# Kernel optimization log

Hardware: AMD Instinct MI355X
Metric: run time of the kernel (lower is better)

Reference implementation:

```python
import jax, jax.numpy as jnp
import numpy as np

ALPHA = 0.2  # LeakyReLU negative slope
NEG_INF = -9e15


def setup_inputs() -> dict:
    key = jax.random.key(0)
    k1, k2, k3, k4 = jax.random.split(key, 4)
    B, N, F_in, F_out = 8, 2048, 256, 128
    h = jax.random.normal(k1, (B, N, F_in), dtype=jnp.float32)
    adj = jax.random.randint(k2, (B, N, N), 0, 2, dtype=jnp.int32)
    # xavier_uniform with gain=1.414
    def xavier(k, shape, gain=1.414):
        fan_in, fan_out = shape[0], shape[1]
        limit = gain * np.sqrt(6.0 / (fan_in + fan_out))
        return jax.random.uniform(k, shape, jnp.float32, -limit, limit)
    W = xavier(k3, (F_in, F_out))
    a = xavier(k4, (2 * F_out, 1))
    return {"h": h, "adj": adj, "W": W, "a": a}


def reference(h, adj, W, a):
    # h: [B,N,F_in], adj: [B,N,N], W: [F_in,F_out], a: [2*F_out,1]
    Wh = jnp.einsum('bnf,fe->bne', h, W)  # [B,N,E]
    E = Wh.shape[-1]
    a_src, a_dst = a[:E, 0], a[E:, 0]
    # e[b,i,j] = leakyrelu(Wh[b,i].a_src + Wh[b,j].a_dst)  (additive decomposition
    # of a @ concat(Wh_i, Wh_j) -- same math, no [B,N,N,2E] intermediate)
    s_src = Wh @ a_src  # [B,N]
    s_dst = Wh @ a_dst  # [B,N]
    e = jax.nn.leaky_relu(s_src[:, :, None] + s_dst[:, None, :], negative_slope=ALPHA)
    e = jnp.where(adj > 0, e, NEG_INF)
    attention = jax.nn.softmax(e, axis=2)  # [B,N,N]
    # dropout p=0.0 / eval mode -> identity
    h_prime = jnp.einsum('bij,bje->bie', attention, Wh)
    return jax.nn.elu(h_prime)  # concat=True
```

## Files before the change

kernel.cpp:

```cpp
#include <hip/hip_runtime.h>
#include <hip/hip_bf16.h>

#define GAT_ALPHA 0.2f
#define LOG2E 1.4426950408889634f

typedef float f32x4 __attribute__((ext_vector_type(4)));
typedef int   i32x4 __attribute__((ext_vector_type(4)));
typedef short bf16x8 __attribute__((ext_vector_type(8)));

static constexpr int Nn  = 2048;
static constexpr int FIN = 256;
static constexpr int FO  = 128;

static __device__ __forceinline__ unsigned short f2bf(float x) {
    __hip_bfloat16 h = __float2bfloat16(x);
    return __builtin_bit_cast(unsigned short, h);
}
static __device__ __forceinline__ float bf2f(unsigned short u) {
    unsigned int v = ((unsigned int)u) << 16;
    return __builtin_bit_cast(float, v);
}

__global__ __launch_bounds__(256) void gat_prep(
        const float* __restrict__ W, const float* __restrict__ a,
        float* __restrict__ wa, unsigned int* __restrict__ md_key)
{
    __shared__ float pr[32][8];
    __shared__ float pd[32][8];
    const int t = threadIdx.x;
    const int kl = t >> 3, seg = t & 7;
    const int k = blockIdx.x * 32 + kl;
    float ps = 0.f, pv = 0.f;
    const float* wr = W + (size_t)k * FO + seg * 16;
    #pragma unroll
    for (int f = 0; f < 16; f += 4) {
        f32x4 wv = *(const f32x4*)(wr + f);
        f32x4 as = *(const f32x4*)(a + seg * 16 + f);
        f32x4 ad = *(const f32x4*)(a + FO + seg * 16 + f);
        ps += wv[0]*as[0] + wv[1]*as[1] + wv[2]*as[2] + wv[3]*as[3];
        pv += wv[0]*ad[0] + wv[1]*ad[1] + wv[2]*ad[2] + wv[3]*ad[3];
    }
    pr[kl][seg] = ps; pd[kl][seg] = pv;
    __syncthreads();
    if (t < 32) {
        float s = 0.f, d = 0.f;
        #pragma unroll
        for (int j = 0; j < 8; ++j) { s += pr[t][j]; d += pd[t][j]; }
        wa[blockIdx.x * 32 + t]       = s;
        wa[256 + blockIdx.x * 32 + t] = d;
    }
    if (blockIdx.x == 0 && t < 8) md_key[t] = 0u;
}

__global__ __launch_bounds__(256) void gat_wh(
        const float* __restrict__ h, const float* __restrict__ W,
        const float* __restrict__ wa, unsigned short* __restrict__ WhB,
        float* __restrict__ s_src, float* __restrict__ s_dst,
        unsigned int* __restrict__ md_key)
{
    __shared__ unsigned short WT[FO][264];
    __shared__ float wal[512];
    __shared__ float sred[64][4][2];
    __shared__ float red64[64];
    const int t  = threadIdx.x;
    const int b  = blockIdx.x & 7;
    const int n0 = (blockIdx.x >> 3) << 6;

    if (t < 128) *(f32x4*)&wal[t * 4] = *(const f32x4*)&wa[t * 4];
    #pragma unroll
    for (int c = 0; c < 32; ++c) {
        int flat = c * 1024 + t * 4;
        int k = flat >> 7, f = flat & 127;
        f32x4 wv = *(const f32x4*)&W[flat];
        WT[f + 0][k] = f2bf(wv[0]);
        WT[f + 1][k] = f2bf(wv[1]);
        WT[f + 2][k] = f2bf(wv[2]);
        WT[f + 3][k] = f2bf(wv[3]);
    }
    __syncthreads();

    {
        const int row = t >> 2, seg = t & 3;
        const float* hp  = h + ((size_t)(b * Nn + n0 + row)) * FIN + seg * 64;
        const float* was = &wal[seg * 64];
        const float* wad = &wal[256 + seg * 64];
        float ps = 0.f, pv = 0.f;
        #pragma unroll
        for (int j = 0; j < 64; j += 4) {
            f32x4 hv = *(const f32x4*)(hp + j);
            f32x4 sv = *(const f32x4*)(was + j);
            f32x4 dv = *(const f32x4*)(wad + j);
            ps += hv[0]*sv[0] + hv[1]*sv[1] + hv[2]*sv[2] + hv[3]*sv[3];
            pv += hv[0]*dv[0] + hv[1]*dv[1] + hv[2]*dv[2] + hv[3]*dv[3];
        }
        sred[row][seg][0] = ps;
        sred[row][seg][1] = pv;
    }
    __syncthreads();
    if (t < 64) {
        float s = sred[t][0][0] + sred[t][1][0] + sred[t][2][0] + sred[t][3][0];
        float d = sred[t][0][1] + sred[t][1][1] + sred[t][2][1] + sred[t][3][1];
        s_src[b * Nn + n0 + t] = s;
        s_dst[b * Nn + n0 + t] = d;
        red64[t] = d;
    }
    __syncthreads();
    if (t < 16) red64[t] = fmaxf(fmaxf(red64[t], red64[t + 16]),
                                 fmaxf(red64[t + 32], red64[t + 48]));
    __syncthreads();
    if (t == 0) {
        float m = red64[0];
        #pragma unroll
        for (int j = 1; j < 16; ++j) m = fmaxf(m, red64[j]);
        unsigned int bits = __builtin_bit_cast(unsigned int, m);
        unsigned int key  = (bits & 0x80000000u) ? ~bits : (bits | 0x80000000u);
        atomicMax(md_key + b, key);
    }

    const int w = t >> 6, lane = t & 63, n16 = lane & 15, quad = lane >> 4;
    const float* ha = h + ((size_t)(b * Nn + n0 + w * 16 + n16)) * FIN + quad * 8;
    f32x4 acc[8] = {};
    #pragma unroll
    for (int ks = 0; ks < 8; ++ks) {
        f32x4 h0 = *(const f32x4*)(ha + ks * 32);
        f32x4 h1 = *(const f32x4*)(ha + ks * 32 + 4);
        bf16x8 af;
        af[0] = (short)f2bf(h0[0]); af[1] = (short)f2bf(h0[1]);
        af[2] = (short)f2bf(h0[2]); af[3] = (short)f2bf(h0[3]);
        af[4] = (short)f2bf(h1[0]); af[5] = (short)f2bf(h1[1]);
        af[6] = (short)f2bf(h1[2]); af[7] = (short)f2bf(h1[3]);
        #pragma unroll
        for (int nt = 0; nt < 8; ++nt) {
            bf16x8 bfr = *(const bf16x8*)&WT[nt * 16 + n16][ks * 32 + quad * 8];
            acc[nt] = __builtin_amdgcn_mfma_f32_16x16x32_bf16(af, bfr, acc[nt], 0, 0, 0);
        }
    }
    {
        const int K   = (n0 >> 5) + (w >> 1);
        const int jl  = ((w & 1) << 4) + (quad << 2);
        const int q2  = jl >> 3;
        const int off = jl & 7;
        unsigned short* wpb = WhB + (((size_t)(b * 64 + K)) << 12)
                                  + (((q2 << 4) + n16) << 3) + off;
        #pragma unroll
        for (int nt = 0; nt < 8; ++nt) {
            ushort4 pk;
            pk.x = f2bf(acc[nt][0]); pk.y = f2bf(acc[nt][1]);
            pk.z = f2bf(acc[nt][2]); pk.w = f2bf(acc[nt][3]);
            *(ushort4*)(wpb + ((size_t)nt << 9)) = pk;
        }
    }
}

__global__ __launch_bounds__(256, 3) void gat_attn(
        const int* __restrict__ adj,
        const unsigned short* __restrict__ WhB,
        const float* __restrict__ s_src, const float* __restrict__ s_dst,
        const unsigned int* __restrict__ md_key, float* __restrict__ out)
{
    __shared__ float sdl[2048];
    __shared__ unsigned long long msk[32][34];
    __shared__ float accbuf[2][32][132];
    __shared__ float l_red[32];

    const int t = threadIdx.x, w = t >> 6, lane = t & 63;
    const int n16 = lane & 15, quad = lane >> 4;
    const int b  = blockIdx.x & 7;
    const int i0 = (blockIdx.x >> 3) << 5;

    {
        const int* ab = adj + ((size_t)(b * Nn + i0)) * Nn;
        unsigned int* mskw = (unsigned int*)&msk[0][0];
        #pragma unroll 2
        for (int s = 0; s < 8; ++s) {
            const int* p = ab + (s << 13) + (t << 5);
            unsigned int m = 0;
            #pragma unroll
            for (int c = 0; c < 8; ++c) {
                i32x4 v = *(const i32x4*)(p + (c << 2));
                m |= (v[0] > 0 ? 1u : 0u) << (c * 4 + 0);
                m |= (v[1] > 0 ? 1u : 0u) << (c * 4 + 1);
                m |= (v[2] > 0 ? 1u : 0u) << (c * 4 + 2);
                m |= (v[3] > 0 ? 1u : 0u) << (c * 4 + 3);
            }
            const int wi = (s << 8) + t;
            mskw[(wi >> 6) * 68 + (wi & 63)] = m;
        }
    }
    #pragma unroll
    for (int c = 0; c < 2; ++c) {
        int idx = (c << 10) + (t << 2);
        *(f32x4*)&sdl[idx] = *(const f32x4*)&s_dst[b * Nn + idx];
    }
    if (t < 32) l_red[t] = 0.f;
    __syncthreads();

    const unsigned int key = md_key[b];
    const unsigned int mb_ = (key & 0x80000000u) ? (key ^ 0x80000000u) : ~key;
    const float mdb = __builtin_bit_cast(float, mb_);
    float ssL[2], mi[2];
    #pragma unroll
    for (int ig = 0; ig < 2; ++ig) {
        float ss = s_src[b * Nn + i0 + (ig << 4) + n16];
        float tm = ss + mdb;
        mi[ig]  = fmaxf(tm, GAT_ALPHA * tm) * LOG2E;
        ssL[ig] = ss * LOG2E;
    }

    const unsigned short* wb = WhB + ((size_t)b << 18) + ((size_t)lane << 3);
    f32x4 acc[2][8] = {};
    float ls0 = 0.f, ls1 = 0.f;

    for (int s = 0; s < 16; ++s) {
        const int ks = (s << 2) | w;
        const int kw = ks << 5;
        const unsigned short* wp = wb + ((size_t)ks << 12);
        bf16x8 bfr[8];
        #pragma unroll
        for (int nt = 0; nt < 8; ++nt)
            bfr[nt] = *(const bf16x8*)(wp + (nt << 9));
        f32x4 d0 = *(const f32x4*)&sdl[kw + (quad << 3)];
        f32x4 d1 = *(const f32x4*)&sdl[kw + (quad << 3) + 4];
        float dv[8] = {d0[0],d0[1],d0[2],d0[3],d1[0],d1[1],d1[2],d1[3]};
        #pragma unroll
        for (int ig = 0; ig < 2; ++ig) {
            unsigned long long m64 = msk[(ig << 4) + n16][kw >> 6];
            unsigned int mh = (kw & 32) ? (unsigned int)(m64 >> 32) : (unsigned int)m64;
            mh >>= (quad << 3);
            bf16x8 af;
            float lsl = 0.f;
            #pragma unroll
            for (int jj = 0; jj < 8; ++jj) {
                float u  = __builtin_fmaf(dv[jj], LOG2E, ssL[ig]);
                float lr = fmaxf(u, GAT_ALPHA * u);
                float e  = __builtin_amdgcn_exp2f(lr - mi[ig]);
                e = ((mh >> jj) & 1u) ? e : 0.f;
                unsigned short ub = f2bf(e);
                af[jj] = (short)ub;
                lsl += bf2f(ub);
            }
            if (ig == 0) ls0 += lsl; else ls1 += lsl;
            #pragma unroll
            for (int nt = 0; nt < 8; ++nt)
                acc[ig][nt] = __builtin_amdgcn_mfma_f32_16x16x32_bf16(af, bfr[nt], acc[ig][nt], 0, 0, 0);
        }
    }

    atomicAdd(&l_red[n16], ls0);
    atomicAdd(&l_red[16 + n16], ls1);
    if (w < 2) {
        #pragma unroll
        for (int ig = 0; ig < 2; ++ig)
            #pragma unroll
            for (int nt = 0; nt < 8; ++nt)
                #pragma unroll
                for (int rr = 0; rr < 4; ++rr)
                    accbuf[w][(ig << 4) + (quad << 2) + rr][(nt << 4) + n16] = acc[ig][nt][rr];
    }
    __syncthreads();
    if (w >= 2) {
        #pragma unroll
        for (int ig = 0; ig < 2; ++ig)
            #pragma unroll
            for (int nt = 0; nt < 8; ++nt)
                #pragma unroll
                for (int rr = 0; rr < 4; ++rr)
                    accbuf[w - 2][(ig << 4) + (quad << 2) + rr][(nt << 4) + n16] += acc[ig][nt][rr];
    }
    __syncthreads();
    float* ob = out + ((size_t)(b * Nn + i0)) * FO;
    #pragma unroll
    for (int c = 0; c < 4; ++c) {
        int flat = (c << 10) + (t << 2);
        int m = flat >> 7, f = flat & 127;
        f32x4 v0 = *(const f32x4*)&accbuf[0][m][f];
        f32x4 v1 = *(const f32x4*)&accbuf[1][m][f];
        float l = l_red[m];
        f32x4 o;
        #pragma unroll
        for (int j = 0; j < 4; ++j) {
            float x = (v0[j] + v1[j]) / l;
            o[j] = x > 0.f ? x : expm1f(x);
        }
        *(f32x4*)&ob[(size_t)m * FO + f] = o;
    }
}

extern "C" void kernel_launch(void* const* d_in, const int* in_sizes, int n_in,
                              void* d_out, int out_size, void* d_ws, size_t ws_size,
                              hipStream_t stream)
{
    const float* h   = (const float*)d_in[0];
    const int*   adj = (const int*)d_in[1];
    const float* W   = (const float*)d_in[2];
    const float* a   = (const float*)d_in[3];
    float* out = (float*)d_out;

    char* ws = (char*)d_ws;
    unsigned short* WhB   = (unsigned short*)ws;
    float* s_src          = (float*)(ws + 8388608);
    float* s_dst          = (float*)(ws + 8454144);
    float* wa             = (float*)(ws + 8519680);
    unsigned int* md_key  = (unsigned int*)(ws + 8521728);

    hipLaunchKernelGGL(gat_prep, dim3(8),   dim3(256), 0, stream, W, a, wa, md_key);
    hipLaunchKernelGGL(gat_wh,   dim3(256), dim3(256), 0, stream, h, W, wa, WhB, s_src, s_dst, md_key);
    hipLaunchKernelGGL(gat_attn, dim3(512), dim3(256), 0, stream, adj, WhB, s_src, s_dst, md_key, out);
}
```

Measured before the change: 243.2 us.

## Fuse prep, Wh projection and attention into one cooperative kernel with grid sync

Replaces the three-kernel pipeline with a single cooperative kernel of 512 blocks. Each block first loads and bit-packs its adjacency rows into shared memory, computes the W·a vectors and its slice of Wh, s_src and s_dst, then does a grid-wide sync before running the masked-softmax attention and aggregation. This removes the separate launches and the small serial prep kernel, and overlaps the large adjacency read with the projection phase. In exchange it needs every block co-resident (launch bounds of 2 blocks per CU and large LDS use), adds a grid barrier and a memset, and falls back to the old kernels if the cooperative launch fails.

```diff
diff --git a/kernel.cpp b/kernel.cpp
--- a/kernel.cpp
+++ b/kernel.cpp
@@ -1,5 +1,8 @@
 #include <hip/hip_runtime.h>
 #include <hip/hip_bf16.h>
+#include <hip/hip_cooperative_groups.h>
+
+namespace cg = cooperative_groups;
 
 #define GAT_ALPHA 0.2f
 #define LOG2E 1.4426950408889634f
@@ -19,6 +22,243 @@
 static __device__ __forceinline__ float bf2f(unsigned short u) {
     unsigned int v = ((unsigned int)u) << 16;
     return __builtin_bit_cast(float, v);
+}
+
+__global__ __launch_bounds__(256, 2) void gat_fused(
+        const float* __restrict__ h, const int* __restrict__ adj,
+        const float* __restrict__ W, const float* __restrict__ a,
+        unsigned short* __restrict__ WhB, float* __restrict__ s_src,
+        float* __restrict__ s_dst, unsigned int* __restrict__ md_key,
+        float* __restrict__ out)
+{
+    __shared__ __align__(16) unsigned short WTbuf[128 * 264];
+    __shared__ unsigned long long msk[32][34];
+    __shared__ float wal[512];
+    __shared__ float sred[32][8][2];
+    __shared__ float red32[32];
+    __shared__ float l_red[32];
+
+    const int t = threadIdx.x, w = t >> 6, lane = t & 63;
+    const int n16 = lane & 15, quad = lane >> 4;
+    const int b  = blockIdx.x & 7;
+    const int i0 = (blockIdx.x >> 3) << 5;
+
+    unsigned short (*WT)[264] = (unsigned short (*)[264])WTbuf;
+    float* sdl = (float*)WTbuf;
+    float (*acb)[132] = (float (*)[132])((float*)WTbuf + 2048);
+
+    {
+        const int* ab = adj + ((size_t)(b * Nn + i0)) * Nn;
+        unsigned int* mskw = (unsigned int*)&msk[0][0];
+        #pragma unroll 2
+        for (int s = 0; s < 8; ++s) {
+            const int* p = ab + (s << 13) + (t << 5);
+            unsigned int m = 0;
+            #pragma unroll
+            for (int c = 0; c < 8; ++c) {
+                i32x4 v = *(const i32x4*)(p + (c << 2));
+                m |= (v[0] > 0 ? 1u : 0u) << (c * 4 + 0);
+                m |= (v[1] > 0 ? 1u : 0u) << (c * 4 + 1);
+                m |= (v[2] > 0 ? 1u : 0u) << (c * 4 + 2);
+                m |= (v[3] > 0 ? 1u : 0u) << (c * 4 + 3);
+            }
+            const int wi = (s << 8) + t;
+            mskw[(wi >> 6) * 68 + (wi & 63)] = m;
+        }
+    }
+    #pragma unroll
+    for (int c = 0; c < 32; ++c) {
+        int flat = c * 1024 + t * 4;
+        int k = flat >> 7, f = flat & 127;
+        f32x4 wv = *(const f32x4*)&W[flat];
+        WT[f + 0][k] = f2bf(wv[0]);
+        WT[f + 1][k] = f2bf(wv[1]);
+        WT[f + 2][k] = f2bf(wv[2]);
+        WT[f + 3][k] = f2bf(wv[3]);
+    }
+    {
+        const float* wr = W + (size_t)t * FO;
+        float ps = 0.f, pv = 0.f;
+        #pragma unroll
+        for (int f = 0; f < FO; f += 4) {
+            f32x4 wv = *(const f32x4*)(wr + f);
+            f32x4 as = *(const f32x4*)(a + f);
+            f32x4 ad = *(const f32x4*)(a + FO + f);
+            ps += wv[0]*as[0] + wv[1]*as[1] + wv[2]*as[2] + wv[3]*as[3];
+            pv += wv[0]*ad[0] + wv[1]*ad[1] + wv[2]*ad[2] + wv[3]*ad[3];
+        }
+        wal[t] = ps; wal[256 + t] = pv;
+    }
+    __syncthreads();
+    {
+        const int r = t >> 3, seg = t & 7;
+        const float* hp  = h + ((size_t)(b * Nn + i0 + r)) * FIN + seg * 32;
+        const float* was = &wal[seg * 32];
+        const float* wad = &wal[256 + seg * 32];
+        float ps = 0.f, pv = 0.f;
+        #pragma unroll
+        for (int j = 0; j < 32; j += 4) {
+            f32x4 hv = *(const f32x4*)(hp + j);
+            f32x4 sv = *(const f32x4*)(was + j);
+            f32x4 dv = *(const f32x4*)(wad + j);
+            ps += hv[0]*sv[0] + hv[1]*sv[1] + hv[2]*sv[2] + hv[3]*sv[3];
+            pv += hv[0]*dv[0] + hv[1]*dv[1] + hv[2]*dv[2] + hv[3]*dv[3];
+        }
+        sred[r][seg][0] = ps;
+        sred[r][seg][1] = pv;
+    }
+    __syncthreads();
+    if (t < 32) {
+        float s = 0.f, d = 0.f;
+        #pragma unroll
+        for (int j = 0; j < 8; ++j) { s += sred[t][j][0]; d += sred[t][j][1]; }
+        s_src[b * Nn + i0 + t] = s;
+        s_dst[b * Nn + i0 + t] = d;
+        red32[t] = d;
+    }
+    __syncthreads();
+    if (t == 0) {
+        float m = red32[0];
+        #pragma unroll
+        for (int j = 1; j < 32; ++j) m = fmaxf(m, red32[j]);
+        unsigned int bits = __builtin_bit_cast(unsigned int, m);
+        unsigned int key  = (bits & 0x80000000u) ? ~bits : (bits | 0x80000000u);
+        atomicMax(md_key + b, key);
+    }
+    {
+        const int rg = (w & 1) << 4;
+        const int fh = (w >> 1) << 2;
+        const float* ha = h + ((size_t)(b * Nn + i0 + rg + n16)) * FIN + quad * 8;
+        f32x4 acc[4] = {};
+        #pragma unroll
+        for (int ks = 0; ks < 8; ++ks) {
+            f32x4 h0 = *(const f32x4*)(ha + ks * 32);
+            f32x4 h1 = *(const f32x4*)(ha + ks * 32 + 4);
+            bf16x8 af;
+            af[0] = (short)f2bf(h0[0]); af[1] = (short)f2bf(h0[1]);
+            af[2] = (short)f2bf(h0[2]); af[3] = (short)f2bf(h0[3]);
+            af[4] = (short)f2bf(h1[0]); af[5] = (short)f2bf(h1[1]);
+            af[6] = (short)f2bf(h1[2]); af[7] = (short)f2bf(h1[3]);
+            #pragma unroll
+            for (int i = 0; i < 4; ++i) {
+                bf16x8 bfr = *(const bf16x8*)&WT[(fh + i) * 16 + n16][ks * 32 + quad * 8];
+                acc[i] = __builtin_amdgcn_mfma_f32_16x16x32_bf16(af, bfr, acc[i], 0, 0, 0);
+            }
+        }
+        const int K   = i0 >> 5;
+        const int jl  = rg + (quad << 2);
+        const int q2  = jl >> 3;
+        const int off = jl & 7;
+        unsigned short* wpb = WhB + (((size_t)(b * 64 + K)) << 12)
+                                  + (((q2 << 4) + n16) << 3) + off;
+        #pragma unroll
+        for (int i = 0; i < 4; ++i) {
+            ushort4 pk;
+            pk.x = f2bf(acc[i][0]); pk.y = f2bf(acc[i][1]);
+            pk.z = f2bf(acc[i][2]); pk.w = f2bf(acc[i][3]);
+            *(ushort4*)(wpb + ((size_t)(fh + i) << 9)) = pk;
+        }
+    }
+
+    cg::this_grid().sync();
+
+    #pragma unroll
+    for (int c = 0; c < 2; ++c) {
+        int idx = (c << 10) + (t << 2);
+        *(f32x4*)&sdl[idx] = *(const f32x4*)&s_dst[b * Nn + idx];
+    }
+    if (t < 32) l_red[t] = 0.f;
+    __syncthreads();
+
+    const unsigned int key = md_key[b];
+    const unsigned int mb_ = (key & 0x80000000u) ? (key ^ 0x80000000u) : ~key;
+    const float mdb = __builtin_bit_cast(float, mb_);
+    float ssL[2], mi[2];
+    #pragma unroll
+    for (int ig = 0; ig < 2; ++ig) {
+        float ss = s_src[b * Nn + i0 + (ig << 4) + n16];
+        float tm = ss + mdb;
+        mi[ig]  = fmaxf(tm, GAT_ALPHA * tm) * LOG2E;
+        ssL[ig] = ss * LOG2E;
+    }
+
+    const unsigned short* wb = WhB + ((size_t)b << 18) + ((size_t)lane << 3);
+    f32x4 acc[2][8] = {};
+    float ls0 = 0.f, ls1 = 0.f;
+
+    for (int s = 0; s < 16; ++s) {
+        const int ks = (s << 2) | w;
+        const int kw = ks << 5;
+        const unsigned short* wp = wb + ((size_t)ks << 12);
+        bf16x8 bfr[8];
+        #pragma unroll
+        for (int nt = 0; nt < 8; ++nt)
+            bfr[nt] = *(const bf16x8*)(wp + (nt << 9));
+        f32x4 d0 = *(const f32x4*)&sdl[kw + (quad << 3)];
+        f32x4 d1 = *(const f32x4*)&sdl[kw + (quad << 3) + 4];
+        float dv[8] = {d0[0],d0[1],d0[2],d0[3],d1[0],d1[1],d1[2],d1[3]};
+        #pragma unroll
+        for (int ig = 0; ig < 2; ++ig) {
+            unsigned long long m64 = msk[(ig << 4) + n16][kw >> 6];
+            unsigned int mh = (kw & 32) ? (unsigned int)(m64 >> 32) : (unsigned int)m64;
+            mh >>= (quad << 3);
+            bf16x8 af;
+            float lsl = 0.f;
+            #pragma unroll
+            for (int jj = 0; jj < 8; ++jj) {
+                float u  = __builtin_fmaf(dv[jj], LOG2E, ssL[ig]);
+                float lr = fmaxf(u, GAT_ALPHA * u);
+                float e  = __builtin_amdgcn_exp2f(lr - mi[ig]);
+                e = ((mh >> jj) & 1u) ? e : 0.f;
+                unsigned short ub = f2bf(e);
+                af[jj] = (short)ub;
+                lsl += bf2f(ub);
+            }
+            if (ig == 0) ls0 += lsl; else ls1 += lsl;
+            #pragma unroll
+            for (int nt = 0; nt < 8; ++nt)
+                acc[ig][nt] = __builtin_amdgcn_mfma_f32_16x16x32_bf16(af, bfr[nt], acc[ig][nt], 0, 0, 0);
+        }
+    }
+
+    atomicAdd(&l_red[n16], ls0);
+    atomicAdd(&l_red[16 + n16], ls1);
+    if (w < 2) {
+        #pragma unroll
+        for (int ig = 0; ig < 2; ++ig)
+            #pragma unroll
+            for (int nt = 0; nt < 8; ++nt)
+                #pragma unroll
+                for (int rr = 0; rr < 4; ++rr)
+                    acb[(w << 5) + (ig << 4) + (quad << 2) + rr][(nt << 4) + n16] = acc[ig][nt][rr];
+    }
+    __syncthreads();
+    if (w >= 2) {
+        #pragma unroll
+        for (int ig = 0; ig < 2; ++ig)
+            #pragma unroll
+            for (int nt = 0; nt < 8; ++nt)
+                #pragma unroll
+                for (int rr = 0; rr < 4; ++rr)
+                    acb[((w - 2) << 5) + (ig << 4) + (quad << 2) + rr][(nt << 4) + n16] += acc[ig][nt][rr];
+    }
+    __syncthreads();
+    float* ob = out + ((size_t)(b * Nn + i0)) * FO;
+    #pragma unroll
+    for (int c = 0; c < 4; ++c) {
+        int flat = (c << 10) + (t << 2);
+        int m = flat >> 7, f = flat & 127;
+        f32x4 v0 = *(const f32x4*)&acb[m][f];
+        f32x4 v1 = *(const f32x4*)&acb[32 + m][f];
+        float l = l_red[m];
+        f32x4 o;
+        #pragma unroll
+        for (int j = 0; j < 4; ++j) {
+            float x = (v0[j] + v1[j]) / l;
+            o[j] = x > 0.f ? x : expm1f(x);
+        }
+        *(f32x4*)&ob[(size_t)m * FO + f] = o;
+    }
 }
 
 __global__ __launch_bounds__(256) void gat_prep(
@@ -78,7 +318,6 @@
         WT[f + 3][k] = f2bf(wv[3]);
     }
     __syncthreads();
-
     {
         const int row = t >> 2, seg = t & 3;
         const float* hp  = h + ((size_t)(b * Nn + n0 + row)) * FIN + seg * 64;
@@ -116,7 +355,6 @@
         unsigned int key  = (bits & 0x80000000u) ? ~bits : (bits | 0x80000000u);
         atomicMax(md_key + b, key);
     }
-
     const int w = t >> 6, lane = t & 63, n16 = lane & 15, quad = lane >> 4;
     const float* ha = h + ((size_t)(b * Nn + n0 + w * 16 + n16)) * FIN + quad * 8;
     f32x4 acc[8] = {};
@@ -303,7 +541,17 @@
     float* wa             = (float*)(ws + 8519680);
     unsigned int* md_key  = (unsigned int*)(ws + 8521728);
 
-    hipLaunchKernelGGL(gat_prep, dim3(8),   dim3(256), 0, stream, W, a, wa, md_key);
-    hipLaunchKernelGGL(gat_wh,   dim3(256), dim3(256), 0, stream, h, W, wa, WhB, s_src, s_dst, md_key);
-    hipLaunchKernelGGL(gat_attn, dim3(512), dim3(256), 0, stream, adj, WhB, s_src, s_dst, md_key, out);
-}
+    hipMemsetAsync(md_key, 0, 32, stream);
+
+    void* args[] = { (void*)&h, (void*)&adj, (void*)&W, (void*)&a,
+                     (void*)&WhB, (void*)&s_src, (void*)&s_dst,
+                     (void*)&md_key, (void*)&out };
+    hipError_t err = hipLaunchCooperativeKernel((const void*)gat_fused,
+                                                dim3(512), dim3(256),
+                                                args, 0, stream);
+    if (err != hipSuccess) {
+        hipLaunchKernelGGL(gat_prep, dim3(8),   dim3(256), 0, stream, W, a, wa, md_key);
+        hipLaunchKernelGGL(gat_wh,   dim3(256), dim3(256), 0, stream, h, W, wa, WhB, s_src, s_dst, md_key);
+        hipLaunchKernelGGL(gat_attn, dim3(512), dim3(256), 0, stream, adj, WhB, s_src, s_dst, md_key, out);
+    }
+}
```

Result: slower. 327.8 us (+34.8%).

## Halve attention row tile to 16 rows, double grid, prefetch sdl/mask

Applied to the files above, without the earlier changes.

The attention kernel now handles 16 query rows per block instead of 32, so the grid doubles to 1024 blocks and launch bounds allow 4 blocks per CU. The per-step s_dst and adjacency-mask LDS reads are software-prefetched one iteration ahead. The aim is more parallelism and occupancy to hide the adj and WhB load latency. The cost is that each WhB tile is now reused by only one row group, so WhB global/L2 traffic doubles.

```diff
diff --git a/kernel.cpp b/kernel.cpp
--- a/kernel.cpp
+++ b/kernel.cpp
@@ -78,7 +78,6 @@
         WT[f + 3][k] = f2bf(wv[3]);
     }
     __syncthreads();
-
     {
         const int row = t >> 2, seg = t & 3;
         const float* hp  = h + ((size_t)(b * Nn + n0 + row)) * FIN + seg * 64;
@@ -116,7 +115,6 @@
         unsigned int key  = (bits & 0x80000000u) ? ~bits : (bits | 0x80000000u);
         atomicMax(md_key + b, key);
     }
-
     const int w = t >> 6, lane = t & 63, n16 = lane & 15, quad = lane >> 4;
     const float* ha = h + ((size_t)(b * Nn + n0 + w * 16 + n16)) * FIN + quad * 8;
     f32x4 acc[8] = {};
@@ -152,27 +150,27 @@
     }
 }
 
-__global__ __launch_bounds__(256, 3) void gat_attn(
+__global__ __launch_bounds__(256, 4) void gat_attn(
         const int* __restrict__ adj,
         const unsigned short* __restrict__ WhB,
         const float* __restrict__ s_src, const float* __restrict__ s_dst,
         const unsigned int* __restrict__ md_key, float* __restrict__ out)
 {
     __shared__ float sdl[2048];
-    __shared__ unsigned long long msk[32][34];
-    __shared__ float accbuf[2][32][132];
-    __shared__ float l_red[32];
+    __shared__ unsigned long long msk[16][34];
+    __shared__ float accbuf[2][16][132];
+    __shared__ float l_red[16];
 
     const int t = threadIdx.x, w = t >> 6, lane = t & 63;
     const int n16 = lane & 15, quad = lane >> 4;
     const int b  = blockIdx.x & 7;
-    const int i0 = (blockIdx.x >> 3) << 5;
+    const int i0 = (blockIdx.x >> 3) << 4;
 
     {
         const int* ab = adj + ((size_t)(b * Nn + i0)) * Nn;
         unsigned int* mskw = (unsigned int*)&msk[0][0];
         #pragma unroll 2
-        for (int s = 0; s < 8; ++s) {
+        for (int s = 0; s < 4; ++s) {
             const int* p = ab + (s << 13) + (t << 5);
             unsigned int m = 0;
             #pragma unroll
@@ -192,85 +190,85 @@
         int idx = (c << 10) + (t << 2);
         *(f32x4*)&sdl[idx] = *(const f32x4*)&s_dst[b * Nn + idx];
     }
-    if (t < 32) l_red[t] = 0.f;
+    if (t < 16) l_red[t] = 0.f;
     __syncthreads();
 
     const unsigned int key = md_key[b];
     const unsigned int mb_ = (key & 0x80000000u) ? (key ^ 0x80000000u) : ~key;
     const float mdb = __builtin_bit_cast(float, mb_);
-    float ssL[2], mi[2];
-    #pragma unroll
-    for (int ig = 0; ig < 2; ++ig) {
-        float ss = s_src[b * Nn + i0 + (ig << 4) + n16];
-        float tm = ss + mdb;
-        mi[ig]  = fmaxf(tm, GAT_ALPHA * tm) * LOG2E;
-        ssL[ig] = ss * LOG2E;
-    }
+    const float ss  = s_src[b * Nn + i0 + n16];
+    const float tm  = ss + mdb;
+    const float mi  = fmaxf(tm, GAT_ALPHA * tm) * LOG2E;
+    const float ssL = ss * LOG2E;
 
     const unsigned short* wb = WhB + ((size_t)b << 18) + ((size_t)lane << 3);
-    f32x4 acc[2][8] = {};
-    float ls0 = 0.f, ls1 = 0.f;
+    f32x4 acc[8] = {};
+    float ls = 0.f;
+
+    int kw0 = w << 5;
+    f32x4 d0 = *(const f32x4*)&sdl[kw0 + (quad << 3)];
+    f32x4 d1 = *(const f32x4*)&sdl[kw0 + (quad << 3) + 4];
+    unsigned long long m64 = msk[n16][kw0 >> 6];
 
     for (int s = 0; s < 16; ++s) {
         const int ks = (s << 2) | w;
-        const int kw = ks << 5;
         const unsigned short* wp = wb + ((size_t)ks << 12);
         bf16x8 bfr[8];
         #pragma unroll
         for (int nt = 0; nt < 8; ++nt)
             bfr[nt] = *(const bf16x8*)(wp + (nt << 9));
-        f32x4 d0 = *(const f32x4*)&sdl[kw + (quad << 3)];
-        f32x4 d1 = *(const f32x4*)&sdl[kw + (quad << 3) + 4];
-        float dv[8] = {d0[0],d0[1],d0[2],d0[3],d1[0],d1[1],d1[2],d1[3]};
-        #pragma unroll
-        for (int ig = 0; ig < 2; ++ig) {
-            unsigned long long m64 = msk[(ig << 4) + n16][kw >> 6];
-            unsigned int mh = (kw & 32) ? (unsigned int)(m64 >> 32) : (unsigned int)m64;
-            mh >>= (quad << 3);
-            bf16x8 af;
-            float lsl = 0.f;
+
+        f32x4 c0 = d0, c1 = d1;
+        unsigned long long cm = m64;
+        {
+            const int kn = ((s < 15) ? (ks + 4) : w) << 5;
+            d0 = *(const f32x4*)&sdl[kn + (quad << 3)];
+            d1 = *(const f32x4*)&sdl[kn + (quad << 3) + 4];
+            m64 = msk[n16][kn >> 6];
+        }
+
+        const int kwc = ks << 5;
+        unsigned int mh = (kwc & 32) ? (unsigned int)(cm >> 32) : (unsigned int)cm;
+        mh >>= (quad << 3);
+        float dv[8] = {c0[0],c0[1],c0[2],c0[3],c1[0],c1[1],c1[2],c1[3]};
+        bf16x8 af;
+        float lsl = 0.f;
+        #pragma unroll
+        for (int jj = 0; jj < 8; ++jj) {
+            float u  = __builtin_fmaf(dv[jj], LOG2E, ssL);
+            float lr = fmaxf(u, GAT_ALPHA * u);
+            float e  = __builtin_amdgcn_exp2f(lr - mi);
+            e = ((mh >> jj) & 1u) ? e : 0.f;
+            unsigned short ub = f2bf(e);
+            af[jj] = (short)ub;
+            lsl += bf2f(ub);
+        }
+        ls += lsl;
+        #pragma unroll
+        for (int nt = 0; nt < 8; ++nt)
+            acc[nt] = __builtin_amdgcn_mfma_f32_16x16x32_bf16(af, bfr[nt], acc[nt], 0, 0, 0);
+    }
+
+    atomicAdd(&l_red[n16], ls);
+    if (w < 2) {
+        #pragma unroll
+        for (int nt = 0; nt < 8; ++nt)
             #pragma unroll
-            for (int jj = 0; jj < 8; ++jj) {
-                float u  = __builtin_fmaf(dv[jj], LOG2E, ssL[ig]);
-                float lr = fmaxf(u, GAT_ALPHA * u);
-                float e  = __builtin_amdgcn_exp2f(lr - mi[ig]);
-                e = ((mh >> jj) & 1u) ? e : 0.f;
-                unsigned short ub = f2bf(e);
-                af[jj] = (short)ub;
-                lsl += bf2f(ub);
-            }
-            if (ig == 0) ls0 += lsl; else ls1 += lsl;
+            for (int rr = 0; rr < 4; ++rr)
+                accbuf[w][(quad << 2) + rr][(nt << 4) + n16] = acc[nt][rr];
+    }
+    __syncthreads();
+    if (w >= 2) {
+        #pragma unroll
+        for (int nt = 0; nt < 8; ++nt)
             #pragma unroll
-            for (int nt = 0; nt < 8; ++nt)
-                acc[ig][nt] = __builtin_amdgcn_mfma_f32_16x16x32_bf16(af, bfr[nt], acc[ig][nt], 0, 0, 0);
-        }
-    }
-
-    atomicAdd(&l_red[n16], ls0);
-    atomicAdd(&l_red[16 + n16], ls1);
-    if (w < 2) {
-        #pragma unroll
-        for (int ig = 0; ig < 2; ++ig)
-            #pragma unroll
-            for (int nt = 0; nt < 8; ++nt)
-                #pragma unroll
-                for (int rr = 0; rr < 4; ++rr)
-                    accbuf[w][(ig << 4) + (quad << 2) + rr][(nt << 4) + n16] = acc[ig][nt][rr];
-    }
-    __syncthreads();
-    if (w >= 2) {
-        #pragma unroll
-        for (int ig = 0; ig < 2; ++ig)
-            #pragma unroll
-            for (int nt = 0; nt < 8; ++nt)
-                #pragma unroll
-                for (int rr = 0; rr < 4; ++rr)
-                    accbuf[w - 2][(ig << 4) + (quad << 2) + rr][(nt << 4) + n16] += acc[ig][nt][rr];
+            for (int rr = 0; rr < 4; ++rr)
+                accbuf[w - 2][(quad << 2) + rr][(nt << 4) + n16] += acc[nt][rr];
     }
     __syncthreads();
     float* ob = out + ((size_t)(b * Nn + i0)) * FO;
     #pragma unroll
-    for (int c = 0; c < 4; ++c) {
+    for (int c = 0; c < 2; ++c) {
         int flat = (c << 10) + (t << 2);
         int m = flat >> 7, f = flat & 127;
         f32x4 v0 = *(const f32x4*)&accbuf[0][m][f];
@@ -303,7 +301,7 @@
     float* wa             = (float*)(ws + 8519680);
     unsigned int* md_key  = (unsigned int*)(ws + 8521728);
 
-    hipLaunchKernelGGL(gat_prep, dim3(8),   dim3(256), 0, stream, W, a, wa, md_key);
-    hipLaunchKernelGGL(gat_wh,   dim3(256), dim3(256), 0, stream, h, W, wa, WhB, s_src, s_dst, md_key);
-    hipLaunchKernelGGL(gat_attn, dim3(512), dim3(256), 0, stream, adj, WhB, s_src, s_dst, md_key, out);
-}
+    hipLaunchKernelGGL(gat_prep, dim3(8),    dim3(256), 0, stream, W, a, wa, md_key);
+    hipLaunchKernelGGL(gat_wh,   dim3(256),  dim3(256), 0, stream, h, W, wa, WhB, s_src, s_dst, md_key);
+    hipLaunchKernelGGL(gat_attn, dim3(1024), dim3(256), 0, stream, adj, WhB, s_src, s_dst, md_key, out);
+}
```

Measured after the change: 240.4 us. About the same (-1.2%).
